# Performance work log

Measured on AMD Instinct MI355X. Metric: run time of the kernel, lower is better.

The kernel has to match this reference:

```python
import jax, jax.numpy as jnp
import numpy as np


def _three_nn(xyz1, xyz2):
    # xyz1: [B,N1,3], xyz2: [B,N2,3]
    # Squared euclidean distances, as in the original three_nn CUDA/TF op.
    d2 = (jnp.sum(xyz1 * xyz1, axis=-1)[:, :, None]
          + jnp.sum(xyz2 * xyz2, axis=-1)[:, None, :]
          - 2.0 * jnp.einsum('bnd,bmd->bnm', xyz1, xyz2))  # [B,N1,N2]
    neg_vals, idx = jax.lax.top_k(-d2, 3)                 # 3 smallest
    return -neg_vals, idx                                  # dist [B,N1,3], idx [B,N1,3]


def reference(xyz1, xyz2, points1, points2, w1, w2):
    dist, idx = _three_nn(xyz1, xyz2)
    dist = jnp.maximum(dist, 1e-10)
    inv = 1.0 / dist                                       # [B,N1,3]
    weight = inv / jnp.sum(inv, axis=2, keepdims=True)     # [B,N1,3]

    B = points2.shape[0]
    b_idx = jnp.arange(B)[:, None, None]
    gathered = points2[b_idx, idx]                         # [B,N1,3,C2]
    interpolated = jnp.einsum('bnk,bnkc->bnc', weight, gathered)  # [B,N1,C2]

    new_points = jnp.concatenate([interpolated, points1], axis=2)  # [B,N1,C2+C1]

    # 1x1 conv MLP = per-point matmul; bn=False, activation=relu on all layers
    h = jax.nn.relu(jnp.einsum('bnc,cf->bnf', new_points, w1))
    h = jax.nn.relu(jnp.einsum('bnc,cf->bnf', h, w2))
    return h


def setup_inputs() -> dict:
    key = jax.random.key(0)
    k1, k2, k3, k4, k5, k6 = jax.random.split(key, 6)
    B, N1, N2, C1, C2 = 4, 8192, 2048, 128, 256
    xyz1 = jax.random.normal(k1, (B, N1, 3), dtype=jnp.float32)
    xyz2 = jax.random.normal(k2, (B, N2, 3), dtype=jnp.float32)
    points1 = jax.random.normal(k3, (B, N1, C1), dtype=jnp.float32)
    points2 = jax.random.normal(k4, (B, N2, C2), dtype=jnp.float32)
    # glorot-normal-ish init for the 1x1 conv kernels
    w1 = jax.random.normal(k5, (C2 + C1, 256), dtype=jnp.float32) * (2.0 / (C2 + C1 + 256)) ** 0.5
    w2 = jax.random.normal(k6, (256, 256), dtype=jnp.float32) * (2.0 / (256 + 256)) ** 0.5
    return {"xyz1": xyz1, "xyz2": xyz2, "points1": points1, "points2": points2, "w1": w1, "w2": w2}
```

## Files before the change

kernel.cpp:

```cpp
#include <hip/hip_runtime.h>
#include <stdint.h>

typedef unsigned short u16;
typedef unsigned int   u32;

#define NB 4
#define N1 8192
#define N2 2048
#define C1 128
#define C2 256
#define KK1 384
#define FF 256
#define TM 64
#define NTHR 1024
#define NCH 16
#define PTSA 768
#define SUBA (PTSA / NCH)
#define PTSB 1280
#define SUBB (PTSB / NCH)
#define TILES_PER_B (N1 / TM)
#define APAD 400
#define HPAD 272
#define NKT1 (KK1 / 32)
#define NKT2 (FF / 32)

typedef short short8 __attribute__((ext_vector_type(8)));
typedef float floatx4 __attribute__((ext_vector_type(4)));
typedef float f32x2  __attribute__((ext_vector_type(2)));
typedef u32   u32x4  __attribute__((ext_vector_type(4)));

union ABFrag { u32 u[4]; short8 v; u32x4 q; };

__device__ __forceinline__ u16 f2b(float f) {
    u32 x = __float_as_uint(f);
    return (u16)((x + 0x7FFFu + ((x >> 16) & 1u)) >> 16);
}
__device__ __forceinline__ u32 pack2(float a, float b) {
    u32 r;
    asm("v_cvt_pk_bf16_f32 %0, %1, %2" : "=v"(r) : "v"(a), "v"(b));
    return r;
}

#define INS3(d, ix, d0, d1, d2, i0, i1, i2)                         \
    {                                                               \
        float n0 = fminf(d, d0);                                    \
        float n1 = __builtin_amdgcn_fmed3f(d, d0, d1);              \
        float n2 = __builtin_amdgcn_fmed3f(d, d1, d2);              \
        bool c0 = d < d0, c1 = d < d1, c2 = d < d2;                 \
        int t01 = c0 ? i0 : ix;                                     \
        i0      = c0 ? ix : i0;                                     \
        int t12 = c1 ? i1 : t01;                                    \
        i1      = c1 ? t01 : i1;                                    \
        i2      = c2 ? t12 : i2;                                    \
        d0 = n0; d1 = n1; d2 = n2;                                  \
    }

__global__ __launch_bounds__(256) void prep_kernel(
    const float* __restrict__ w1, const float* __restrict__ w2,
    const float* __restrict__ xyz2,
    u32x4* __restrict__ w1F, u32x4* __restrict__ w2F, float* __restrict__ xq)
{
    int i = blockIdx.x * 256 + threadIdx.x;
    if (i < 16 * NKT1 * 64) {
        int nt = i / (NKT1 * 64), rem = i % (NKT1 * 64);
        int kt = rem / 64, lane = rem % 64;
        int n  = nt * 16 + (lane & 15);
        int k0 = kt * 32 + (lane >> 4) * 8;
        const float* wc = w1 + n;
        ABFrag f;
        f.u[0] = pack2(wc[(k0 + 0) * FF], wc[(k0 + 1) * FF]);
        f.u[1] = pack2(wc[(k0 + 2) * FF], wc[(k0 + 3) * FF]);
        f.u[2] = pack2(wc[(k0 + 4) * FF], wc[(k0 + 5) * FF]);
        f.u[3] = pack2(wc[(k0 + 6) * FF], wc[(k0 + 7) * FF]);
        w1F[i] = f.q;
        return;
    }
    i -= 16 * NKT1 * 64;
    if (i < 16 * NKT2 * 64) {
        int nt = i / (NKT2 * 64), rem = i % (NKT2 * 64);
        int kt = rem / 64, lane = rem % 64;
        int n  = nt * 16 + (lane & 15);
        int k0 = kt * 32 + (lane >> 4) * 8;
        const float* wc = w2 + n;
        ABFrag f;
        f.u[0] = pack2(wc[(k0 + 0) * FF], wc[(k0 + 1) * FF]);
        f.u[1] = pack2(wc[(k0 + 2) * FF], wc[(k0 + 3) * FF]);
        f.u[2] = pack2(wc[(k0 + 4) * FF], wc[(k0 + 5) * FF]);
        f.u[3] = pack2(wc[(k0 + 6) * FF], wc[(k0 + 7) * FF]);
        w2F[i] = f.q;
        return;
    }
    i -= 16 * NKT2 * 64;
    if (i < NB * N2) {
        const float* q = xyz2 + (size_t)i * 3;
        float x = q[0], y = q[1], z = q[2];
        float s2 = __fadd_rn(__fadd_rn(__fmul_rn(x,x), __fmul_rn(y,y)), __fmul_rn(z,z));
        int p = i >> 1, e = i & 1;
        float* rec = xq + (size_t)p * 8;
        rec[0 + e] = -2.0f * x;
        rec[2 + e] = -2.0f * y;
        rec[4 + e] = -2.0f * z;
        rec[6 + e] = s2;
    }
}

__global__ __launch_bounds__(NTHR, 8) void fp_fused_kernel(
    const float* __restrict__ xyz1, const float* __restrict__ p1,
    const float* __restrict__ p2,
    const u32x4* __restrict__ w1F,  const u32x4* __restrict__ w2F,
    const float4* __restrict__ xq,  float* __restrict__ out)
{
    __shared__ int   s_idx[TM][3];
    __shared__ float s_wt[TM][3];
    __shared__ float s_m[TM][8];
    __shared__ float s_pd[NCH * TM * 3];
    __shared__ int   s_pi[NCH * TM * 3];
    __shared__ __align__(16) char s_buf[TM * APAD * 2];

    const int tid = threadIdx.x;
    const int b   = blockIdx.x / TILES_PER_B;
    const int t0  = (blockIdx.x % TILES_PER_B) * TM;
    u16* A = (u16*)s_buf;

    const int c4 = (tid & 31) * 4, r32 = tid >> 5;
    float4 pv0 = *(const float4*)(p1 + ((size_t)b * N1 + t0 + r32) * C1 + c4);
    float4 pv1 = *(const float4*)(p1 + ((size_t)b * N1 + t0 + r32 + 32) * C1 + c4);

    const int r  = tid & 63;
    const int ch = __builtin_amdgcn_readfirstlane(tid >> 6);

    const float* q = xyz1 + ((size_t)b * N1 + t0 + r) * 3;
    const float qx = q[0], qy = q[1], qz = q[2];
    const float s1 = __fadd_rn(__fadd_rn(__fmul_rn(qx,qx), __fmul_rn(qy,qy)), __fmul_rn(qz,qz));

    {
        const float4* cb = xq + ((size_t)b * (N2 / 2) + ch * (SUBA / 2)) * 2;
        float bd0 = 3e38f, bd1 = 3e38f, bd2 = 3e38f;
        int   bi0 = -1, bi1 = -1, bi2 = -1;
        const int j0 = ch * SUBA;
        #pragma unroll 8
        for (int jj = 0; jj < SUBA / 2; ++jj) {
            float4 f0 = cb[2 * jj];
            float4 f1 = cb[2 * jj + 1];
            f32x2 dpair;
            {
                #pragma clang fp contract(off)
                f32x2 qx2 = {qx, qx}, qy2 = {qy, qy}, qz2 = {qz, qz}, s1v = {s1, s1};
                f32x2 nx = {f0.x, f0.y}, ny = {f0.z, f0.w};
                f32x2 nz = {f1.x, f1.y}, ss = {f1.z, f1.w};
                f32x2 u  = qx2 * nx;
                f32x2 v  = qy2 * ny;
                f32x2 w  = u + v;
                f32x2 z2 = qz2 * nz;
                f32x2 t  = w + z2;
                f32x2 s12 = s1v + ss;
                dpair = s12 + t;
            }
            #pragma unroll
            for (int e = 0; e < 2; ++e) {
                float d = dpair[e];
                int   j = j0 + 2 * jj + e;
                INS3(d, j, bd0, bd1, bd2, bi0, bi1, bi2);
            }
        }
        const int o = (ch * TM + r) * 3;
        s_pd[o+0] = bd0; s_pd[o+1] = bd1; s_pd[o+2] = bd2;
        s_pi[o+0] = bi0; s_pi[o+1] = bi1; s_pi[o+2] = bi2;
    }

    {
        u32* w0 = (u32*)(A + r32 * APAD + 256 + c4);
        w0[0] = pack2(pv0.x, pv0.y);
        w0[1] = pack2(pv0.z, pv0.w);
        u32* w1p = (u32*)(A + (r32 + 32) * APAD + 256 + c4);
        w1p[0] = pack2(pv1.x, pv1.y);
        w1p[1] = pack2(pv1.z, pv1.w);
    }
    __syncthreads();

    if (tid < 256) {
        const int row = tid & 63, grp = tid >> 6;
        float d0 = 3e38f, d1 = 3e38f, d2 = 3e38f;
        int   i0 = -1, i1 = -1, i2 = -1;
        #pragma unroll
        for (int c = 0; c < 4; ++c) {
            const int o = ((grp * 4 + c) * TM + row) * 3;
            #pragma unroll
            for (int k = 0; k < 3; ++k) {
                float d = s_pd[o + k]; int ix = s_pi[o + k];
                INS3(d, ix, d0, d1, d2, i0, i1, i2);
            }
        }
        float* sg = (float*)(s_buf + row * (APAD * 2) + grp * 32);
        sg[0] = d0; sg[1] = d1; sg[2] = d2;
        sg[3] = __int_as_float(i0); sg[4] = __int_as_float(i1); sg[5] = __int_as_float(i2);
    }
    __syncthreads();

    if (tid < TM) {
        float d0 = 3e38f, d1 = 3e38f, d2 = 3e38f;
        int   i0 = -1, i1 = -1, i2 = -1;
        #pragma unroll
        for (int g = 0; g < 4; ++g) {
            const float* sg = (const float*)(s_buf + tid * (APAD * 2) + g * 32);
            #pragma unroll
            for (int k = 0; k < 3; ++k) {
                float d = sg[k]; int ix = __float_as_int(sg[3 + k]);
                INS3(d, ix, d0, d1, d2, i0, i1, i2);
            }
        }
        s_m[tid][0] = d0; s_m[tid][1] = d1; s_m[tid][2] = d2;
        s_m[tid][4] = __int_as_float(i0);
        s_m[tid][5] = __int_as_float(i1);
        s_m[tid][6] = __int_as_float(i2);
    }
    __syncthreads();

    {
        const float bound = s_m[r][2];
        const float4* cb = xq + ((size_t)b * (N2 / 2) + (PTSA / 2) + ch * (SUBB / 2)) * 2;
        float bd0 = bound, bd1 = bound, bd2 = bound;
        int   bi0 = -1, bi1 = -1, bi2 = -1;
        const int j0 = PTSA + ch * SUBB;
        #pragma unroll 4
        for (int jj = 0; jj < SUBB / 2; ++jj) {
            float4 f0 = cb[2 * jj];
            float4 f1 = cb[2 * jj + 1];
            f32x2 dpair;
            {
                #pragma clang fp contract(off)
                f32x2 qx2 = {qx, qx}, qy2 = {qy, qy}, qz2 = {qz, qz}, s1v = {s1, s1};
                f32x2 nx = {f0.x, f0.y}, ny = {f0.z, f0.w};
                f32x2 nz = {f1.x, f1.y}, ss = {f1.z, f1.w};
                f32x2 u  = qx2 * nx;
                f32x2 v  = qy2 * ny;
                f32x2 w  = u + v;
                f32x2 z2 = qz2 * nz;
                f32x2 t  = w + z2;
                f32x2 s12 = s1v + ss;
                dpair = s12 + t;
            }
            if (__any((dpair.x < bd2) || (dpair.y < bd2))) {
                #pragma unroll
                for (int e = 0; e < 2; ++e) {
                    float d = dpair[e];
                    int   j = j0 + 2 * jj + e;
                    INS3(d, j, bd0, bd1, bd2, bi0, bi1, bi2);
                }
            }
        }
        const int o = (ch * TM + r) * 3;
        s_pd[o+0] = bd0; s_pd[o+1] = bd1; s_pd[o+2] = bd2;
        s_pi[o+0] = bi0; s_pi[o+1] = bi1; s_pi[o+2] = bi2;
    }
    __syncthreads();

    if (tid < 256) {
        const int row = tid & 63, grp = tid >> 6;
        float d0 = 3e38f, d1 = 3e38f, d2 = 3e38f;
        int   i0 = -1, i1 = -1, i2 = -1;
        #pragma unroll
        for (int c = 0; c < 4; ++c) {
            const int o = ((grp * 4 + c) * TM + row) * 3;
            #pragma unroll
            for (int k = 0; k < 3; ++k) {
                float d = s_pd[o + k]; int ix = s_pi[o + k];
                INS3(d, ix, d0, d1, d2, i0, i1, i2);
            }
        }
        float* sg = (float*)(s_buf + row * (APAD * 2) + grp * 32);
        sg[0] = d0; sg[1] = d1; sg[2] = d2;
        sg[3] = __int_as_float(i0); sg[4] = __int_as_float(i1); sg[5] = __int_as_float(i2);
    }
    __syncthreads();

    if (tid < TM) {
        float d0 = s_m[tid][0], d1 = s_m[tid][1], d2 = s_m[tid][2];
        int   i0 = __float_as_int(s_m[tid][4]);
        int   i1 = __float_as_int(s_m[tid][5]);
        int   i2 = __float_as_int(s_m[tid][6]);
        #pragma unroll
        for (int g = 0; g < 4; ++g) {
            const float* sg = (const float*)(s_buf + tid * (APAD * 2) + g * 32);
            #pragma unroll
            for (int k = 0; k < 3; ++k) {
                float d = sg[k]; int ix = __float_as_int(sg[3 + k]);
                INS3(d, ix, d0, d1, d2, i0, i1, i2);
            }
        }
        d0 = fmaxf(d0, 1e-10f); d1 = fmaxf(d1, 1e-10f); d2 = fmaxf(d2, 1e-10f);
        float v0 = 1.0f / d0, v1 = 1.0f / d1, v2 = 1.0f / d2;
        float s  = 1.0f / (v0 + v1 + v2);
        s_wt[tid][0] = v0 * s; s_wt[tid][1] = v1 * s; s_wt[tid][2] = v2 * s;
        s_idx[tid][0] = i0; s_idx[tid][1] = i1; s_idx[tid][2] = i2;
    }
    __syncthreads();

    {
        const float* pb = p2 + (size_t)b * N2 * C2;
        const int col4 = (tid & 63) * 4;
        const int wvr  = tid >> 6;
        float4 a0[2], a1[2], a2[2];
        {
            int rr = wvr;
            a0[0] = *(const float4*)(pb + (size_t)s_idx[rr][0] * C2 + col4);
            a1[0] = *(const float4*)(pb + (size_t)s_idx[rr][1] * C2 + col4);
            a2[0] = *(const float4*)(pb + (size_t)s_idx[rr][2] * C2 + col4);
        }
        #pragma unroll
        for (int m = 0; m < 4; ++m) {
            int cur = m & 1, nxt = cur ^ 1;
            if (m < 3) {
                int rn = wvr + (m + 1) * 16;
                a0[nxt] = *(const float4*)(pb + (size_t)s_idx[rn][0] * C2 + col4);
                a1[nxt] = *(const float4*)(pb + (size_t)s_idx[rn][1] * C2 + col4);
                a2[nxt] = *(const float4*)(pb + (size_t)s_idx[rn][2] * C2 + col4);
            }
            int rr = wvr + m * 16;
            float w0 = s_wt[rr][0], w1v = s_wt[rr][1], w2v = s_wt[rr][2];
            float e0 = w0 * a0[cur].x + w1v * a1[cur].x + w2v * a2[cur].x;
            float e1 = w0 * a0[cur].y + w1v * a1[cur].y + w2v * a2[cur].y;
            float e2 = w0 * a0[cur].z + w1v * a1[cur].z + w2v * a2[cur].z;
            float e3 = w0 * a0[cur].w + w1v * a1[cur].w + w2v * a2[cur].w;
            u32* w = (u32*)(A + rr * APAD + col4);
            w[0] = pack2(e0, e1);
            w[1] = pack2(e2, e3);
        }
    }
    __syncthreads();

    const int lane = tid & 63;
    const int wv   = tid >> 6;
    const int lr   = lane & 15;
    const int lg   = lane >> 4;
    const int kb8  = lg * 8;
    const int wvb  = wv * 16;

    int id1[4], id2[4];
    {
        u16 rbf = f2b((float)lr);
        u16 c32 = f2b(1.0f / 32.0f);
        ABFrag pa, pc;
        u32 ra = (u32)rbf | ((u32)rbf << 16);
        u32 rc = (u32)c32 | ((u32)c32 << 16);
        pa.u[0] = pa.u[1] = pa.u[2] = pa.u[3] = ra;
        pc.u[0] = pc.u[1] = pc.u[2] = pc.u[3] = rc;
        floatx4 z = {0.f, 0.f, 0.f, 0.f};
        floatx4 D1 = __builtin_amdgcn_mfma_f32_16x16x32_bf16(pa.v, pc.v, z, 0, 0, 0);
        floatx4 D2 = __builtin_amdgcn_mfma_f32_16x16x32_bf16(pc.v, pa.v, z, 0, 0, 0);
        #pragma unroll
        for (int g = 0; g < 4; ++g) { id1[g] = (int)(D1[g] + 0.5f); id2[g] = (int)(D2[g] + 0.5f); }
    }

    floatx4 acc[4];
    #pragma unroll
    for (int i = 0; i < 4; ++i) acc[i] = floatx4{0.f, 0.f, 0.f, 0.f};
    {
        const u32x4* wf = w1F + (size_t)(wv * NKT1) * 64 + lane;
        ABFrag bfc; bfc.q = wf[0];
        #pragma unroll 2
        for (int kk = 0; kk < NKT1; ++kk) {
            ABFrag bfn;
            bfn.q = wf[(size_t)((kk + 1 < NKT1) ? kk + 1 : kk) * 64];
            ABFrag a[4];
            #pragma unroll
            for (int rt = 0; rt < 4; ++rt)
                a[rt].q = *(const u32x4*)(A + (rt * 16 + lr) * APAD + kk * 32 + kb8);
            #pragma unroll
            for (int rt = 0; rt < 4; ++rt)
                acc[rt] = __builtin_amdgcn_mfma_f32_16x16x32_bf16(a[rt].v, bfc.v, acc[rt], 0, 0, 0);
            bfc = bfn;
        }
    }
    __syncthreads();

    u16* H = (u16*)s_buf;
    #pragma unroll
    for (int rt = 0; rt < 4; ++rt)
        #pragma unroll
        for (int g = 0; g < 4; ++g) {
            int row = rt * 16 + id1[g];
            int col = wvb + id2[g];
            H[row * HPAD + col] = f2b(fmaxf(acc[rt][g], 0.0f));
        }
    __syncthreads();

    floatx4 acc2[4];
    #pragma unroll
    for (int i = 0; i < 4; ++i) acc2[i] = floatx4{0.f, 0.f, 0.f, 0.f};
    {
        const u32x4* wf = w2F + (size_t)(wv * NKT2) * 64 + lane;
        ABFrag bfc; bfc.q = wf[0];
        #pragma unroll 2
        for (int kk = 0; kk < NKT2; ++kk) {
            ABFrag bfn;
            bfn.q = wf[(size_t)((kk + 1 < NKT2) ? kk + 1 : kk) * 64];
            ABFrag a[4];
            #pragma unroll
            for (int rt = 0; rt < 4; ++rt)
                a[rt].q = *(const u32x4*)(H + (rt * 16 + lr) * HPAD + kk * 32 + kb8);
            #pragma unroll
            for (int rt = 0; rt < 4; ++rt)
                acc2[rt] = __builtin_amdgcn_mfma_f32_16x16x32_bf16(a[rt].v, bfc.v, acc2[rt], 0, 0, 0);
            bfc = bfn;
        }
    }

    float* ob = out + ((size_t)b * N1 + t0) * FF;
    #pragma unroll
    for (int rt = 0; rt < 4; ++rt)
        #pragma unroll
        for (int g = 0; g < 4; ++g) {
            int row = rt * 16 + id1[g];
            int col = wvb + id2[g];
            ob[(size_t)row * FF + col] = fmaxf(acc2[rt][g], 0.0f);
        }
}

extern "C" void kernel_launch(void* const* d_in, const int* in_sizes, int n_in,
                              void* d_out, int out_size, void* d_ws, size_t ws_size,
                              hipStream_t stream)
{
    (void)in_sizes; (void)n_in; (void)out_size; (void)ws_size;
    const float* xyz1 = (const float*)d_in[0];
    const float* xyz2 = (const float*)d_in[1];
    const float* p1   = (const float*)d_in[2];
    const float* p2   = (const float*)d_in[3];
    const float* w1   = (const float*)d_in[4];
    const float* w2   = (const float*)d_in[5];
    float* out = (float*)d_out;

    u32x4* w1F = (u32x4*)d_ws;
    u32x4* w2F = w1F + 16 * NKT1 * 64;
    float* xqw = (float*)(w2F + 16 * NKT2 * 64);

    int prep_items = 16 * NKT1 * 64 + 16 * NKT2 * 64 + NB * N2;
    prep_kernel<<<(prep_items + 255) / 256, 256, 0, stream>>>(w1, w2, xyz2, w1F, w2F, xqw);
    fp_fused_kernel<<<NB * TILES_PER_B, NTHR, 0, stream>>>(
        xyz1, p1, p2, w1F, w2F, (const float4*)xqw, out);
}
```

Measured before the change: 57.75 us.

## Stage weight transpose via LDS in prep, prefetch candidates and weight fragments early

```diff
diff --git a/kernel.cpp b/kernel.cpp
--- a/kernel.cpp
+++ b/kernel.cpp
@@ -18,6 +18,7 @@
 #define SUBA (PTSA / NCH)
 #define PTSB 1280
 #define SUBB (PTSB / NCH)
+#define NPRE 8
 #define TILES_PER_B (N1 / TM)
 #define APAD 400
 #define HPAD 272
@@ -55,53 +56,64 @@
         d0 = n0; d1 = n1; d2 = n2;                                  \
     }
 
-__global__ __launch_bounds__(256) void prep_kernel(
+#define DPAIR(f0, f1, qx, qy, qz, s1, out)                          \
+    {                                                               \
+        _Pragma("clang fp contract(off)")                           \
+        f32x2 qx2 = {qx, qx}, qy2 = {qy, qy}, qz2 = {qz, qz};       \
+        f32x2 s1v = {s1, s1};                                       \
+        f32x2 nx = {f0.x, f0.y}, ny = {f0.z, f0.w};                 \
+        f32x2 nz = {f1.x, f1.y}, ss = {f1.z, f1.w};                 \
+        f32x2 u  = qx2 * nx;                                        \
+        f32x2 v  = qy2 * ny;                                        \
+        f32x2 w  = u + v;                                           \
+        f32x2 z2 = qz2 * nz;                                        \
+        f32x2 t  = w + z2;                                          \
+        f32x2 s12 = s1v + ss;                                       \
+        out = s12 + t;                                              \
+    }
+
+__global__ __launch_bounds__(1024) void prep_kernel(
     const float* __restrict__ w1, const float* __restrict__ w2,
     const float* __restrict__ xyz2,
     u32x4* __restrict__ w1F, u32x4* __restrict__ w2F, float* __restrict__ xq)
 {
-    int i = blockIdx.x * 256 + threadIdx.x;
-    if (i < 16 * NKT1 * 64) {
-        int nt = i / (NKT1 * 64), rem = i % (NKT1 * 64);
-        int kt = rem / 64, lane = rem % 64;
-        int n  = nt * 16 + (lane & 15);
-        int k0 = kt * 32 + (lane >> 4) * 8;
-        const float* wc = w1 + n;
+    __shared__ float lds[32][257];
+    const int tid = threadIdx.x;
+    const int blk = blockIdx.x;
+
+    if (blk < NKT1 + NKT2) {
+        const bool isw1 = blk < NKT1;
+        const int  kt   = isw1 ? blk : blk - NKT1;
+        const float* src = (isw1 ? w1 : w2) + (size_t)kt * 32 * FF;
+        #pragma unroll
+        for (int i = 0; i < 8; ++i) {
+            int e = tid + i * 1024;
+            lds[e >> 8][e & 255] = src[e];
+        }
+        __syncthreads();
+        const int nt = tid >> 6, lane = tid & 63;
+        const int n  = nt * 16 + (lane & 15);
+        const int k0 = (lane >> 4) * 8;
         ABFrag f;
-        f.u[0] = pack2(wc[(k0 + 0) * FF], wc[(k0 + 1) * FF]);
-        f.u[1] = pack2(wc[(k0 + 2) * FF], wc[(k0 + 3) * FF]);
-        f.u[2] = pack2(wc[(k0 + 4) * FF], wc[(k0 + 5) * FF]);
-        f.u[3] = pack2(wc[(k0 + 6) * FF], wc[(k0 + 7) * FF]);
-        w1F[i] = f.q;
+        f.u[0] = pack2(lds[k0 + 0][n], lds[k0 + 1][n]);
+        f.u[1] = pack2(lds[k0 + 2][n], lds[k0 + 3][n]);
+        f.u[2] = pack2(lds[k0 + 4][n], lds[k0 + 5][n]);
+        f.u[3] = pack2(lds[k0 + 6][n], lds[k0 + 7][n]);
+        if (isw1) w1F[(size_t)(nt * NKT1 + kt) * 64 + lane] = f.q;
+        else      w2F[(size_t)(nt * NKT2 + kt) * 64 + lane] = f.q;
         return;
     }
-    i -= 16 * NKT1 * 64;
-    if (i < 16 * NKT2 * 64) {
-        int nt = i / (NKT2 * 64), rem = i % (NKT2 * 64);
-        int kt = rem / 64, lane = rem % 64;
-        int n  = nt * 16 + (lane & 15);
-        int k0 = kt * 32 + (lane >> 4) * 8;
-        const float* wc = w2 + n;
-        ABFrag f;
-        f.u[0] = pack2(wc[(k0 + 0) * FF], wc[(k0 + 1) * FF]);
-        f.u[1] = pack2(wc[(k0 + 2) * FF], wc[(k0 + 3) * FF]);
-        f.u[2] = pack2(wc[(k0 + 4) * FF], wc[(k0 + 5) * FF]);
-        f.u[3] = pack2(wc[(k0 + 6) * FF], wc[(k0 + 7) * FF]);
-        w2F[i] = f.q;
-        return;
-    }
-    i -= 16 * NKT2 * 64;
-    if (i < NB * N2) {
-        const float* q = xyz2 + (size_t)i * 3;
-        float x = q[0], y = q[1], z = q[2];
-        float s2 = __fadd_rn(__fadd_rn(__fmul_rn(x,x), __fmul_rn(y,y)), __fmul_rn(z,z));
-        int p = i >> 1, e = i & 1;
-        float* rec = xq + (size_t)p * 8;
-        rec[0 + e] = -2.0f * x;
-        rec[2 + e] = -2.0f * y;
-        rec[4 + e] = -2.0f * z;
-        rec[6 + e] = s2;
-    }
+
+    int i = (blk - NKT1 - NKT2) * 1024 + tid;
+    const float* q = xyz2 + (size_t)i * 3;
+    float x = q[0], y = q[1], z = q[2];
+    float s2 = __fadd_rn(__fadd_rn(__fmul_rn(x,x), __fmul_rn(y,y)), __fmul_rn(z,z));
+    int p = i >> 1, e = i & 1;
+    float* rec = xq + (size_t)p * 8;
+    rec[0 + e] = -2.0f * x;
+    rec[2 + e] = -2.0f * y;
+    rec[4 + e] = -2.0f * z;
+    rec[6 + e] = s2;
 }
 
 __global__ __launch_bounds__(NTHR, 8) void fp_fused_kernel(
@@ -143,19 +155,7 @@
             float4 f0 = cb[2 * jj];
             float4 f1 = cb[2 * jj + 1];
             f32x2 dpair;
-            {
-                #pragma clang fp contract(off)
-                f32x2 qx2 = {qx, qx}, qy2 = {qy, qy}, qz2 = {qz, qz}, s1v = {s1, s1};
-                f32x2 nx = {f0.x, f0.y}, ny = {f0.z, f0.w};
-                f32x2 nz = {f1.x, f1.y}, ss = {f1.z, f1.w};
-                f32x2 u  = qx2 * nx;
-                f32x2 v  = qy2 * ny;
-                f32x2 w  = u + v;
-                f32x2 z2 = qz2 * nz;
-                f32x2 t  = w + z2;
-                f32x2 s12 = s1v + ss;
-                dpair = s12 + t;
-            }
+            DPAIR(f0, f1, qx, qy, qz, s1, dpair);
             #pragma unroll
             for (int e = 0; e < 2; ++e) {
                 float d = dpair[e];
@@ -166,6 +166,15 @@
         const int o = (ch * TM + r) * 3;
         s_pd[o+0] = bd0; s_pd[o+1] = bd1; s_pd[o+2] = bd2;
         s_pi[o+0] = bi0; s_pi[o+1] = bi1; s_pi[o+2] = bi2;
+    }
+
+    const float4* cbB = xq + ((size_t)b * (N2 / 2) + (PTSA / 2) + ch * (SUBB / 2)) * 2;
+    f32x2 preB[NPRE];
+    #pragma unroll
+    for (int jj = 0; jj < NPRE; ++jj) {
+        float4 f0 = cbB[2 * jj];
+        float4 f1 = cbB[2 * jj + 1];
+        DPAIR(f0, f1, qx, qy, qz, s1, preB[jj]);
     }
 
     {
@@ -218,28 +227,12 @@
 
     {
         const float bound = s_m[r][2];
-        const float4* cb = xq + ((size_t)b * (N2 / 2) + (PTSA / 2) + ch * (SUBB / 2)) * 2;
         float bd0 = bound, bd1 = bound, bd2 = bound;
         int   bi0 = -1, bi1 = -1, bi2 = -1;
         const int j0 = PTSA + ch * SUBB;
-        #pragma unroll 4
-        for (int jj = 0; jj < SUBB / 2; ++jj) {
-            float4 f0 = cb[2 * jj];
-            float4 f1 = cb[2 * jj + 1];
-            f32x2 dpair;
-            {
-                #pragma clang fp contract(off)
-                f32x2 qx2 = {qx, qx}, qy2 = {qy, qy}, qz2 = {qz, qz}, s1v = {s1, s1};
-                f32x2 nx = {f0.x, f0.y}, ny = {f0.z, f0.w};
-                f32x2 nz = {f1.x, f1.y}, ss = {f1.z, f1.w};
-                f32x2 u  = qx2 * nx;
-                f32x2 v  = qy2 * ny;
-                f32x2 w  = u + v;
-                f32x2 z2 = qz2 * nz;
-                f32x2 t  = w + z2;
-                f32x2 s12 = s1v + ss;
-                dpair = s12 + t;
-            }
+        #pragma unroll
+        for (int jj = 0; jj < NPRE; ++jj) {
+            f32x2 dpair = preB[jj];
             if (__any((dpair.x < bd2) || (dpair.y < bd2))) {
                 #pragma unroll
                 for (int e = 0; e < 2; ++e) {
@@ -249,6 +242,21 @@
                 }
             }
         }
+        #pragma unroll 4
+        for (int jj = NPRE; jj < SUBB / 2; ++jj) {
+            float4 f0 = cbB[2 * jj];
+            float4 f1 = cbB[2 * jj + 1];
+            f32x2 dpair;
+            DPAIR(f0, f1, qx, qy, qz, s1, dpair);
+            if (__any((dpair.x < bd2) || (dpair.y < bd2))) {
+                #pragma unroll
+                for (int e = 0; e < 2; ++e) {
+                    float d = dpair[e];
+                    int   j = j0 + 2 * jj + e;
+                    INS3(d, j, bd0, bd1, bd2, bi0, bi1, bi2);
+                }
+            }
+        }
         const int o = (ch * TM + r) * 3;
         s_pd[o+0] = bd0; s_pd[o+1] = bd1; s_pd[o+2] = bd2;
         s_pi[o+0] = bi0; s_pi[o+1] = bi1; s_pi[o+2] = bi2;
@@ -295,6 +303,16 @@
         s_idx[tid][0] = i0; s_idx[tid][1] = i1; s_idx[tid][2] = i2;
     }
     __syncthreads();
+
+    const int lane = tid & 63;
+    const int wv   = tid >> 6;
+    const int lr   = lane & 15;
+    const int lg   = lane >> 4;
+    const int kb8  = lg * 8;
+    const int wvb  = wv * 16;
+    const u32x4* wf1 = w1F + (size_t)(wv * NKT1) * 64 + lane;
+    const u32x4* wf2 = w2F + (size_t)(wv * NKT2) * 64 + lane;
+    ABFrag bfc1; bfc1.q = wf1[0];
 
     {
         const float* pb = p2 + (size_t)b * N2 * C2;
@@ -328,13 +346,6 @@
         }
     }
     __syncthreads();
-
-    const int lane = tid & 63;
-    const int wv   = tid >> 6;
-    const int lr   = lane & 15;
-    const int lg   = lane >> 4;
-    const int kb8  = lg * 8;
-    const int wvb  = wv * 16;
 
     int id1[4], id2[4];
     {
@@ -356,22 +367,21 @@
     #pragma unroll
     for (int i = 0; i < 4; ++i) acc[i] = floatx4{0.f, 0.f, 0.f, 0.f};
     {
-        const u32x4* wf = w1F + (size_t)(wv * NKT1) * 64 + lane;
-        ABFrag bfc; bfc.q = wf[0];
         #pragma unroll 2
         for (int kk = 0; kk < NKT1; ++kk) {
             ABFrag bfn;
-            bfn.q = wf[(size_t)((kk + 1 < NKT1) ? kk + 1 : kk) * 64];
+            bfn.q = wf1[(size_t)((kk + 1 < NKT1) ? kk + 1 : kk) * 64];
             ABFrag a[4];
             #pragma unroll
             for (int rt = 0; rt < 4; ++rt)
                 a[rt].q = *(const u32x4*)(A + (rt * 16 + lr) * APAD + kk * 32 + kb8);
             #pragma unroll
             for (int rt = 0; rt < 4; ++rt)
-                acc[rt] = __builtin_amdgcn_mfma_f32_16x16x32_bf16(a[rt].v, bfc.v, acc[rt], 0, 0, 0);
-            bfc = bfn;
-        }
-    }
+                acc[rt] = __builtin_amdgcn_mfma_f32_16x16x32_bf16(a[rt].v, bfc1.v, acc[rt], 0, 0, 0);
+            bfc1 = bfn;
+        }
+    }
+    ABFrag bfc2; bfc2.q = wf2[0];
     __syncthreads();
 
     u16* H = (u16*)s_buf;
@@ -389,20 +399,18 @@
     #pragma unroll
     for (int i = 0; i < 4; ++i) acc2[i] = floatx4{0.f, 0.f, 0.f, 0.f};
     {
-        const u32x4* wf = w2F + (size_t)(wv * NKT2) * 64 + lane;
-        ABFrag bfc; bfc.q = wf[0];
         #pragma unroll 2
         for (int kk = 0; kk < NKT2; ++kk) {
             ABFrag bfn;
-            bfn.q = wf[(size_t)((kk + 1 < NKT2) ? kk + 1 : kk) * 64];
+            bfn.q = wf2[(size_t)((kk + 1 < NKT2) ? kk + 1 : kk) * 64];
             ABFrag a[4];
             #pragma unroll
             for (int rt = 0; rt < 4; ++rt)
                 a[rt].q = *(const u32x4*)(H + (rt * 16 + lr) * HPAD + kk * 32 + kb8);
             #pragma unroll
             for (int rt = 0; rt < 4; ++rt)
-                acc2[rt] = __builtin_amdgcn_mfma_f32_16x16x32_bf16(a[rt].v, bfc.v, acc2[rt], 0, 0, 0);
-            bfc = bfn;
+                acc2[rt] = __builtin_amdgcn_mfma_f32_16x16x32_bf16(a[rt].v, bfc2.v, acc2[rt], 0, 0, 0);
+            bfc2 = bfn;
         }
     }
 
@@ -434,8 +442,8 @@
     u32x4* w2F = w1F + 16 * NKT1 * 64;
     float* xqw = (float*)(w2F + 16 * NKT2 * 64);
 
-    int prep_items = 16 * NKT1 * 64 + 16 * NKT2 * 64 + NB * N2;
-    prep_kernel<<<(prep_items + 255) / 256, 256, 0, stream>>>(w1, w2, xyz2, w1F, w2F, xqw);
+    prep_kernel<<<NKT1 + NKT2 + (NB * N2 / 1024), 1024, 0, stream>>>(
+        w1, w2, xyz2, w1F, w2F, xqw);
     fp_fused_kernel<<<NB * TILES_PER_B, NTHR, 0, stream>>>(
         xyz1, p1, p2, w1F, w2F, (const float4*)xqw, out);
 }
```

After: 58.76 us. About the same (+1.7%).
